# Performance work log

Hardware: AMD Instinct MI355X
Metric: run time of the kernel (lower is better)

Reference implementation:

```python
import jax, jax.numpy as jnp
import numpy as np

# ---- static hyperparameters (mirror init_kwargs) ----
L_MAX = 3
N_MAX_L = [8, 6, 4, 2]            # radial basis size per l (precomputer.n_max_l)
N_CHANNELS = 32                   # num_element_channels
K_MAX_L = [n * N_CHANNELS for n in N_MAX_L]   # [256, 192, 128, 64]
SH_SIZES = [2 * l + 1 for l in range(L_MAX + 1)]  # [1,3,5,7]
MP_SCALING = 0.1
NU_SCALING = 0.1
NU_MAX = 2                        # max_correlation_order_per_layer
N_LAYERS = 2                      # num_message_passing_layers

# Fixed CG coupling tensors for all valid (l1, l2, L) with |l1-l2|<=L<=min(l1+l2, L_MAX).
# (Deterministic stand-ins for real Clebsch-Gordan coefficients; same sparsity/coupling
# structure and identical in fwd and fwdbwd modules.)
_rng = np.random.RandomState(0)
CG = {}
for _l1 in range(L_MAX + 1):
    for _l2 in range(L_MAX + 1):
        for _L in range(abs(_l1 - _l2), min(_l1 + _l2, L_MAX) + 1):
            CG[(_l1, _l2, _L)] = jnp.asarray(
                (_rng.randn(2 * _l1 + 1, 2 * _l2 + 1, 2 * _L + 1) * 0.2).astype(np.float32))


def split_l(x, sizes):
    out, i = [], 0
    for s in sizes:
        out.append(x[:, i:i + s])
        i += s
    return out


def embed_centers(feats, emb):
    # feats[l]: [N, 2l+1, n_l*C]; multiply channel block c by per-atom embedding emb[:, c]
    C = emb.shape[1]
    out = []
    for f in feats:
        n, m, k = f.shape
        out.append((f.reshape(n, m, k // C, C) * emb[:, None, None, :]).reshape(n, m, k))
    return out


def tensor_product(A, B):
    # per-atom CG tensor product, channel-aligned with truncation to min k
    n = A[0].shape[0]
    out = [jnp.zeros((n, 2 * L + 1, K_MAX_L[L]), A[0].dtype) for L in range(L_MAX + 1)]
    for (l1, l2, L), cg in CG.items():
        kk = min(K_MAX_L[l1], K_MAX_L[l2], K_MAX_L[L])
        t = jnp.einsum('nak,nbk,abM->nMk', A[l1][:, :, :kk], B[l2][:, :, :kk], cg)
        out[L] = out[L].at[:, :, :kk].add(t)
    return out


def cg_iterate(feats):
    # CGIterator: nu_max-1 iterated tensor products with residual accumulation
    g = feats
    for _ in range(NU_MAX - 1):
        tp = tensor_product(g, feats)
        g = [g[l] + NU_SCALING * tp[l] for l in range(L_MAX + 1)]
    return g


def invariant_mp(rb_l, sh_l, centers, emb_nbr, n_atoms):
    # spherical expansion: scatter rb x sh x neighbor-embedding over pairs -> centers
    out = []
    for l in range(L_MAX + 1):
        # [P, 2l+1, n_l, C] -> [P, 2l+1, k_l]
        msg = sh_l[l][:, :, None, None] * rb_l[l][:, None, :, None] * emb_nbr[:, None, None, :]
        msg = msg.reshape(msg.shape[0], 2 * l + 1, -1)
        out.append(MP_SCALING * jax.ops.segment_sum(msg, centers, num_segments=n_atoms))
    return out


def equivariant_mp(rb_l, sh_l, centers, neighbors, feats, n_atoms):
    # pair messages: CG-couple radially weighted SH edge features with neighbor features
    edge = [sh_l[l] * rb_l[l].sum(-1, keepdims=True) for l in range(L_MAX + 1)]  # [P, 2l+1]
    out = [jnp.zeros((n_atoms, 2 * L + 1, K_MAX_L[L]), feats[0].dtype) for L in range(L_MAX + 1)]
    for (l1, l2, L), cg in CG.items():
        kk = min(K_MAX_L[l2], K_MAX_L[L])
        w = jnp.einsum('pa,abM->pbM', edge[l1], cg)        # [P, 2l2+1, 2L+1]
        fg = feats[l2][neighbors, :, :kk]                   # gather: [P, 2l2+1, kk]
        msg = jnp.einsum('pbM,pbk->pMk', w, fg)             # [P, 2L+1, kk]
        out[L] = out[L].at[:, :, :kk].add(
            MP_SCALING * jax.ops.segment_sum(msg, centers, num_segments=n_atoms))
    return out


def setup_inputs() -> dict:
    key = jax.random.key(0)
    ks = jax.random.split(key, 8)
    N, P = 5000, 100000
    return {
        'sh': jax.random.normal(ks[0], (P, sum(SH_SIZES)), dtype=jnp.float32),
        'rb': jax.random.uniform(ks[1], (P, sum(N_MAX_L)), dtype=jnp.float32),
        'emb_table': jax.random.normal(ks[2], (4, N_CHANNELS), dtype=jnp.float32),
        'w_energy': jax.random.normal(ks[3], (K_MAX_L[0], 1), dtype=jnp.float32) * 0.05,
        'b_energy': jax.random.normal(ks[4], (1,), dtype=jnp.float32),
        'species_idx': jax.random.randint(ks[5], (N,), 0, 4, dtype=jnp.int32),
        'centers': jax.random.randint(ks[6], (P,), 0, N, dtype=jnp.int32),
        'neighbors': jax.random.randint(ks[7], (P,), 0, N, dtype=jnp.int32),
    }


def reference(sh, rb, emb_table, w_energy, b_energy, species_idx, centers, neighbors):
    n_atoms = species_idx.shape[0]
    sh_l = split_l(sh * NU_SCALING, SH_SIZES)   # nu_scaling applied to spherical harmonics
    rb_l = split_l(rb, N_MAX_L)
    center_emb = emb_table[species_idx]          # [N, C]
    emb_nbr = center_emb[neighbors]              # [P, C]
    # invariant message passing -> spherical expansion, then first CG iteration
    feats = invariant_mp(rb_l, sh_l, centers, emb_nbr, n_atoms)
    feats = cg_iterate(feats)
    # remaining equivariant message-passing layers
    for _ in range(N_LAYERS - 1):
        ef = embed_centers(feats, center_emb)
        mp = equivariant_mp(rb_l, sh_l, centers, neighbors, ef, n_atoms)
        feats = cg_iterate(mp)
    feats = embed_centers(feats, center_emb)
    energies = feats[0] @ w_energy + b_energy    # [N, 1, 1]
    return energies
```

## Files before the change

kernel.cpp:

```cpp
#include <hip/hip_runtime.h>
#include <vector>
#include <cmath>
#include <cstdint>

constexpr int KLc[4]  = {256,192,128,64};
constexpr int NMLc[4] = {8,6,4,2};
constexpr int SHBc[5] = {0,1,4,9,16};
constexpr int RBBc[5] = {0,8,14,18,20};
constexpr int FBc[5]  = {0,256,832,1472,1920};
constexpr int NCMB = 34, CGTOT = 3436, FTOT = 1920;

struct Combos { int l1[NCMB], l2[NCMB], L[NCMB], cgoff[NCMB], kk[NCMB]; };
constexpr Combos make_combos(){
  Combos c{}; int n=0, cg=0;
  for(int a=0;a<=3;a++)for(int b=0;b<=3;b++){
    int lo=a>b?a-b:b-a, hi=(a+b<3)?(a+b):3;
    for(int L=lo;L<=hi;L++){
      c.l1[n]=a; c.l2[n]=b; c.L[n]=L; c.cgoff[n]=cg;
      int mx=a>b?a:b; if(L>mx) mx=L; c.kk[n]=KLc[mx];
      cg+=(2*a+1)*(2*b+1)*(2*L+1); n++;
    }
  }
  return c;
}
constexpr Combos CB = make_combos();
static_assert(CB.cgoff[NCMB-1] + 7*7*7 == CGTOT, "cg size");

struct Grp { int cnt[4]; int list[4][12]; };
constexpr Grp make_Lg(){ Grp g{}; for(int i=0;i<NCMB;i++){ int L=CB.L[i]; g.list[L][g.cnt[L]++]=i; } return g; }
constexpr Grp LG = make_Lg();

struct Rows { int sh[64], rb[64], off[64]; };
constexpr Rows make_rows(){ Rows r{}; int i=0;
  for(int l=0;l<4;l++)for(int m=0;m<2*l+1;m++)for(int n=0;n<NMLc[l];n++){
    r.sh[i]=SHBc[l]+m; r.rb[i]=RBBc[l]+n; r.off[i]=FBc[l]+m*KLc[l]+n*32; i++; }
  for(;i<64;i++){ r.sh[i]=0; r.rb[i]=0; r.off[i]=0; }
  return r; }
constexpr Rows RWS = make_rows();

constexpr int NSL=425, MAXS=107, MAXR=12, RPAD=149;

constexpr int iabs_(int x){ return x<0?-x:x; }
__host__ __device__ constexpr bool sl_valid(int l1,int l2,int kt){ return l2<=3-kt && iabs_(l1-l2)<=3-kt; }

__host__ __device__ constexpr int rb_base(int kt,int l1,int l2){
  int base=0;
  for(int p=0;p<4;p++)for(int q=0;q<4;q++){
    if(p==l1 && q==l2) return base;
    if(sl_valid(p,q,kt)) base += (2*p+1)*(2*q+1);
  }
  return base;
}

struct EqTab {
  int ns[4];
  unsigned char eidx[4][MAXS];
  unsigned char fidx[4][MAXS];
  short         srow[4][MAXS];
  unsigned char sph [4][MAXS];
  int nr[4];
  short roff[4][MAXR];
  int total;
};
constexpr EqTab make_eqtab(){
  EqTab T{}; int gidx=0;
  for(int l2=0;l2<4;l2++)for(int kt=0;kt<4-l2;kt++)for(int b=0;b<2*l2+1;b++){
    const int rowoff = FBc[l2] + b*KLc[l2] + kt*64;
    for(int l1=0;l1<4;l1++){
      if(!sl_valid(l1,l2,kt)) continue;
      for(int a=0;a<2*l1+1;a++){
        int g = (gidx*4)/NSL;
        int s = T.ns[g]++;
        T.eidx[g][s] = (unsigned char)(SHBc[l1]+a);
        int rbi = rb_base(kt,l1,l2) + a*(2*l2+1) + b;
        int ph, sr;
        if(kt==0){ if(l1<=2){ ph=0; sr=rbi; } else { ph=1; sr=rbi-144; } }
        else { ph=kt+1; sr=rbi; }
        T.sph[g][s]=(unsigned char)ph; T.srow[g][s]=(short)sr;
        int ri=-1;
        for(int r=0;r<T.nr[g];r++) if(T.roff[g][r]==(short)rowoff) ri=r;
        if(ri<0){ ri=T.nr[g]; T.roff[g][T.nr[g]++]=(short)rowoff; }
        T.fidx[g][s]=(unsigned char)ri;
        gidx++;
      }
    }
  }
  T.total=gidx;
  return T;
}
constexpr EqTab ET = make_eqtab();
static_assert(ET.total==NSL, "slice count");
static_assert(ET.ns[0]<=MAXS && ET.ns[1]<=MAXS && ET.ns[2]<=MAXS && ET.ns[3]<=MAXS, "MAXS");
static_assert(ET.nr[0]<=MAXR && ET.nr[1]<=MAXR && ET.nr[2]<=MAXR && ET.nr[3]<=MAXR, "MAXR");

struct CAsg { int cnt[4]; unsigned char ci[4][16]; };
constexpr CAsg make_casg(){
  CAsg C{}; bool used[NCMB]{}; int load[4]{};
  for(int it=0; it<NCMB; it++){
    int best=-1, bc=-1;
    for(int i=0;i<NCMB;i++) if(!used[i]){
      int c=(2*CB.l1[i]+1)*(2*CB.l2[i]+1)*(2*CB.L[i]+1);
      if(c>bc){bc=c;best=i;}
    }
    used[best]=true;
    int g=0; for(int j=1;j<4;j++) if(load[j]<load[g]) g=j;
    C.ci[g][C.cnt[g]++]=(unsigned char)best; load[g]+=bc;
  }
  return C;
}
constexpr CAsg CA = make_casg();
static_assert(CA.cnt[0]<=16 && CA.cnt[1]<=16 && CA.cnt[2]<=16 && CA.cnt[3]<=16, "CA cap");

__host__ __device__ constexpr bool combo_in_phase(int ci,int ph){
  int l1=CB.l1[ci], l2=CB.l2[ci], L=CB.L[ci];
  if(ph==0) return l1<=2;
  if(ph==1) return l1==3;
  int kt=ph-1;
  return (l2<=3-kt) && (L<=3-kt);
}
__host__ __device__ constexpr int phase_kt(int ph){ return ph<=1?0:ph-1; }
__host__ __device__ constexpr int phase_rbadj(int ph){ return ph==1?144:0; }

namespace nprng {
struct MT {
  uint32_t mt[624]; int mti; bool has_g; double g;
  void seed(uint32_t s){ for(int i=0;i<624;i++){ mt[i]=s; s=1812433253u*(s^(s>>30))+(uint32_t)i+1u; } mti=624; has_g=false; g=0.0; }
  uint32_t u32(){
    if(mti>=624){
      for(int i=0;i<624;i++){
        uint32_t y=(mt[i]&0x80000000u)|(mt[(i+1)%624]&0x7fffffffu);
        mt[i]=mt[(i+397)%624]^(y>>1)^((y&1u)?0x9908b0dfu:0u);
      }
      mti=0;
    }
    uint32_t y=mt[mti++];
    y^=y>>11; y^=(y<<7)&0x9d2c5680u; y^=(y<<15)&0xefc60000u; y^=y>>18;
    return y;
  }
  double dbl(){ uint32_t a=u32()>>5, b=u32()>>6; return (a*67108864.0+b)/9007199254740992.0; }
  double gauss(){
    if(has_g){ has_g=false; return g; }
    double f,x1,x2,r2;
    do{ x1=2.0*dbl()-1.0; x2=2.0*dbl()-1.0; r2=x1*x1+x2*x2; }while(r2>=1.0||r2==0.0);
    f=sqrt(-2.0*log(r2)/r2);
    g=f*x1; has_g=true; return f*x2;
  }
};
}
static std::vector<float> build_cg(){
  nprng::MT r; r.seed(0);
  std::vector<float> v; v.reserve(CGTOT);
  for(int l1=0;l1<=3;l1++)for(int l2=0;l2<=3;l2++){
    int lo = l1>l2? l1-l2 : l2-l1;
    int hi = (l1+l2<3)? (l1+l2) : 3;
    for(int L=lo;L<=hi;L++){
      int n=(2*l1+1)*(2*l2+1)*(2*L+1);
      for(int i=0;i<n;i++) v.push_back((float)(r.gauss()*0.2));
    }
  }
  return v;
}

__global__ __launch_bounds__(256) void k_cemb(const float* __restrict__ emb_table,
    const int* __restrict__ species, float* __restrict__ cemb, int* __restrict__ counts, int N){
  int i = blockIdx.x*256 + threadIdx.x;
  if(i < N) counts[i] = 0;
  if(i < N*32){ int n = i>>5, c = i&31; cemb[i] = emb_table[species[n]*32 + c]; }
}

__global__ __launch_bounds__(256) void k_hist(const int* __restrict__ centers, int* counts, int P){
  int i = blockIdx.x*256 + threadIdx.x;
  if(i < P) atomicAdd(&counts[centers[i]], 1);
}

__global__ __launch_bounds__(256) void k_scan(const int* __restrict__ counts,
    int* __restrict__ offsets, int* __restrict__ cursor, int N){
  __shared__ int part[256];
  const int t = threadIdx.x;
  const int CH = (N + 255)/256;
  const int lo = t*CH;
  int hi = (t+1)*CH; if(hi > N) hi = N;
  int s = 0;
  for(int i=lo;i<hi;i++) s += counts[i];
  part[t] = s; __syncthreads();
  const int own = s;
  for(int d=1; d<256; d<<=1){
    int v = (t>=d)? part[t-d] : 0;
    __syncthreads();
    part[t] += v;
    __syncthreads();
  }
  int run = part[t] - own;
  for(int i=lo;i<hi;i++){ offsets[i]=run; cursor[i]=run; run += counts[i]; }
  if(t==255) offsets[N] = part[255];
}

__global__ __launch_bounds__(256) void k_scatter(const int* __restrict__ centers,
    int* cursor, int* __restrict__ perm, int P){
  int i = blockIdx.x*256 + threadIdx.x;
  if(i < P){ int c = centers[i]; int pos = atomicAdd(&cursor[c], 1); perm[pos] = i; }
}

__global__ __launch_bounds__(256) void k_inv(const float* __restrict__ sh, const float* __restrict__ rb,
    const float* __restrict__ cemb, const int* __restrict__ nbrs, const int* __restrict__ offsets,
    const int* __restrict__ perm, float* __restrict__ feats){
  const int a = blockIdx.x, t = threadIdx.x;
  __shared__ float sh_s[8][16], rb_s[8][20], emb_s[8][32], shrb_s[8][60];
  const int c = t & 31, rg = t >> 5;
  float acc[8];
  #pragma unroll
  for(int j=0;j<8;j++) acc[j] = 0.f;
  const int beg = offsets[a], cnt = offsets[a+1]-beg;
  for(int jb=0; jb<cnt; jb+=8){
    __syncthreads();
    for(int u=t; u<8*36; u+=256){
      int j=u/36, i=u-36*j;
      if(jb+j<cnt){
        int p=perm[beg+jb+j];
        if(i<16) sh_s[j][i]=sh[p*16+i]*0.1f;
        else     rb_s[j][i-16]=rb[p*20+i-16];
      }
    }
    for(int u=t; u<8*32; u+=256){
      int j=u>>5, i=u&31;
      if(jb+j<cnt){ int nb=nbrs[perm[beg+jb+j]]; emb_s[j][i]=cemb[(size_t)nb*32+i]; }
    }
    __syncthreads();
    for(int u=t; u<8*60; u+=256){
      int j=u/60, r=u-60*j;
      if(jb+j<cnt) shrb_s[j][r] = sh_s[j][RWS.sh[r]] * rb_s[j][RWS.rb[r]];
    }
    __syncthreads();
    const int jm = (cnt-jb<8)?(cnt-jb):8;
    for(int j=0;j<jm;j++){
      const float e = emb_s[j][c];
      #pragma unroll
      for(int q=0;q<8;q++){ int r=rg+8*q; if(r<60) acc[q]=fmaf(shrb_s[j][r], e, acc[q]); }
    }
  }
  #pragma unroll
  for(int q=0;q<8;q++){
    int r = rg + 8*q;
    if(r < 60) feats[(size_t)a*FTOT + RWS.off[r] + c] = 0.1f * acc[q];
  }
}

__global__ __launch_bounds__(256) void k_tp(float* __restrict__ feats, const float* __restrict__ cg){
  const int a = blockIdx.x, t = threadIdx.x;
  __shared__ float f_s[FTOT];
  __shared__ float cg_s[CGTOT];
  float* fa = feats + (size_t)a*FTOT;
  for(int i=t;i<CGTOT;i+=256) cg_s[i] = cg[i];
  for(int i=t;i<FTOT;i+=256)  f_s[i]  = fa[i];
  __syncthreads();
  #pragma unroll
  for(int L=0; L<4; L++){
    const int KLL = KLc[L], nL = 2*L+1;
    const int nel = nL*KLL;
    for(int e=t; e<nel; e+=256){
      const int M = e / KLL, k = e - M*KLL;
      float acc = 0.f;
      #pragma unroll
      for(int gi=0; gi<LG.cnt[L]; gi++){
        const int ci = LG.list[L][gi];
        const int l1 = CB.l1[ci], l2 = CB.l2[ci];
        if(k < CB.kk[ci]){
          const int n2 = 2*l2+1;
          #pragma unroll
          for(int aa=0; aa<2*l1+1; aa++){
            const float Av = f_s[FBc[l1] + aa*KLc[l1] + k];
            #pragma unroll
            for(int b=0; b<n2; b++)
              acc += cg_s[CB.cgoff[ci] + (aa*n2+b)*nL + M] * (Av * f_s[FBc[l2] + b*KLc[l2] + k]);
          }
        }
      }
      fa[FBc[L] + M*KLL + k] = f_s[FBc[L] + M*KLL + k] + 0.1f*acc;
    }
  }
}

template<int G,int PH,int U>
__device__ __forceinline__ void contract_combos(const float* __restrict__ stageT,
    float* __restrict__ out_s, const float* __restrict__ cg, int lane){
  if constexpr (U < CA.cnt[G]) {
    constexpr int ci = CA.ci[G][U];
    if constexpr (combo_in_phase(ci,PH)) {
      constexpr int l1=CB.l1[ci], l2=CB.l2[ci], L=CB.L[ci];
      constexpr int n1=2*l1+1, n2=2*l2+1, nL=2*L+1;
      constexpr int kt=phase_kt(PH);
      constexpr int rbase = rb_base(kt,l1,l2) - phase_rbadj(PH);
      float oa[nL];
      #pragma unroll
      for(int M=0;M<nL;M++) oa[M]=0.f;
      #pragma unroll
      for(int aa=0;aa<n1;aa++){
        #pragma unroll
        for(int b=0;b<n2;b++){
          const float sv = stageT[lane*RPAD + rbase + aa*n2 + b];
          #pragma unroll
          for(int M=0;M<nL;M++)
            oa[M] = fmaf(cg[CB.cgoff[ci] + (aa*n2+b)*nL + M], sv, oa[M]);
        }
      }
      #pragma unroll
      for(int M=0;M<nL;M++)
        atomicAdd(&out_s[FBc[L] + M*KLc[L] + kt*64 + lane], oa[M]);
    }
    contract_combos<G,PH,U+1>(stageT,out_s,cg,lane);
  }
}

template<int G,int PH>
__device__ __forceinline__ void eq_phase(const float* acc, float* stageT, float* out_s,
    const float* __restrict__ cg, int lane){
  __syncthreads();
  #pragma unroll
  for(int s=0;s<ET.ns[G];s++){
    if(ET.sph[G][s]==PH) stageT[lane*RPAD + ET.srow[G][s]] = acc[s];
  }
  __syncthreads();
  contract_combos<G,PH,0>(stageT,out_s,cg,lane);
}

template<int G>
__device__ __forceinline__ void eq_group_main(
    const int a, const int t, const int lane,
    const float* __restrict__ sh, const float* __restrict__ rb,
    const float* __restrict__ cemb, const int* __restrict__ nbrs,
    const int* __restrict__ offsets, const int* __restrict__ perm,
    const float* __restrict__ featsA, float* __restrict__ featsB,
    const float* __restrict__ cg,
    float* stageT, float* out_s, float* edge_s, int* nb_s){
  constexpr int NS = ET.ns[G], NR = ET.nr[G];
  float acc[NS];
  #pragma unroll
  for(int s=0;s<NS;s++) acc[s]=0.f;
  for(int i=t;i<FTOT;i+=256) out_s[i]=0.f;
  const int beg = offsets[a], cnt = offsets[a+1]-beg;
  for(int jb=0; jb<cnt; jb+=8){
    __syncthreads();
    if(t < 128){
      int j=t>>4, i=t&15;
      if(jb+j<cnt){
        int p = perm[beg+jb+j];
        if(i==0) nb_s[j] = nbrs[p];
        int l = (i==0)?0:(i<4)?1:(i<9)?2:3;
        float s=0.f;
        for(int n=RBBc[l]; n<RBBc[l+1]; n++) s += rb[p*20+n];
        edge_s[j*16+i] = sh[p*16+i]*0.1f*s;
      }
    }
    __syncthreads();
    const int jm = (cnt-jb<8)?(cnt-jb):8;
    for(int j=0;j<jm;j++){
      const int nb = nb_s[j];
      const float ce = cemb[(size_t)nb*32 + (lane&31)];
      const float* fp = featsA + (size_t)nb*FTOT + lane;
      float fgv[NR];
      #pragma unroll
      for(int r=0;r<NR;r++) fgv[r] = fp[ET.roff[G][r]] * ce;
      float ed[16];
      #pragma unroll
      for(int q=0;q<4;q++){
        float4 v = *(const float4*)(edge_s + j*16 + q*4);
        ed[q*4]=v.x; ed[q*4+1]=v.y; ed[q*4+2]=v.z; ed[q*4+3]=v.w;
      }
      #pragma unroll
      for(int s=0;s<NS;s++)
        acc[s] = fmaf(ed[ET.eidx[G][s]], fgv[ET.fidx[G][s]], acc[s]);
    }
  }
  eq_phase<G,0>(acc,stageT,out_s,cg,lane);
  eq_phase<G,1>(acc,stageT,out_s,cg,lane);
  eq_phase<G,2>(acc,stageT,out_s,cg,lane);
  eq_phase<G,3>(acc,stageT,out_s,cg,lane);
  eq_phase<G,4>(acc,stageT,out_s,cg,lane);
  __syncthreads();
  float* ob = featsB + (size_t)a*FTOT;
  for(int i=t;i<FTOT;i+=256) ob[i] = 0.1f*out_s[i];
}

__global__ __launch_bounds__(256,3) void k_eq2(const float* __restrict__ sh, const float* __restrict__ rb,
    const float* __restrict__ cemb, const int* __restrict__ nbrs, const int* __restrict__ offsets,
    const int* __restrict__ perm, const float* __restrict__ featsA, float* __restrict__ featsB,
    const float* __restrict__ cg){
  __shared__ float stageT[64*RPAD];
  __shared__ float out_s[FTOT];
  __shared__ float edge_s[8*16];
  __shared__ int   nb_s[8];
  const int a = blockIdx.x, t = threadIdx.x, lane = t&63, g = t>>6;
  switch(g){
    case 0: eq_group_main<0>(a,t,lane,sh,rb,cemb,nbrs,offsets,perm,featsA,featsB,cg,stageT,out_s,edge_s,nb_s); break;
    case 1: eq_group_main<1>(a,t,lane,sh,rb,cemb,nbrs,offsets,perm,featsA,featsB,cg,stageT,out_s,edge_s,nb_s); break;
    case 2: eq_group_main<2>(a,t,lane,sh,rb,cemb,nbrs,offsets,perm,featsA,featsB,cg,stageT,out_s,edge_s,nb_s); break;
    default: eq_group_main<3>(a,t,lane,sh,rb,cemb,nbrs,offsets,perm,featsA,featsB,cg,stageT,out_s,edge_s,nb_s); break;
  }
}

__global__ __launch_bounds__(256) void k_energy(const float* __restrict__ feats,
    const float* __restrict__ cemb, const float* __restrict__ wE, const float* __restrict__ bE,
    float* __restrict__ out, int N){
  const int wid = threadIdx.x >> 6, lane = threadIdx.x & 63;
  const int a = blockIdx.x*4 + wid;
  if(a >= N) return;
  const float e = cemb[(size_t)a*32 + (lane & 31)];
  float s = 0.f;
  for(int k=lane; k<256; k+=64) s += feats[(size_t)a*FTOT + k] * e * wE[k];
  #pragma unroll
  for(int off=32; off; off>>=1) s += __shfl_down(s, off, 64);
  if(lane == 0) out[a] = s + bE[0];
}

extern "C" void kernel_launch(void* const* d_in, const int* in_sizes, int n_in,
                              void* d_out, int out_size, void* d_ws, size_t ws_size,
                              hipStream_t stream){
  const float* sh        = (const float*)d_in[0];
  const float* rb        = (const float*)d_in[1];
  const float* emb_table = (const float*)d_in[2];
  const float* wE        = (const float*)d_in[3];
  const float* bE        = (const float*)d_in[4];
  const int*   species   = (const int*)d_in[5];
  const int*   centers   = (const int*)d_in[6];
  const int*   nbrs      = (const int*)d_in[7];
  const int N = in_sizes[5];
  const int P = in_sizes[6];

  char* ws = (char*)d_ws; size_t off = 0;
  auto carve = [&](size_t bytes)->void*{
    void* p = ws + off; off = (off + bytes + 255) & ~(size_t)255; return p;
  };
  float* cg_d    = (float*)carve((size_t)CGTOT*4);
  float* cemb    = (float*)carve((size_t)N*32*4);
  int*   counts  = (int*)  carve((size_t)N*4);
  int*   offsets = (int*)  carve((size_t)(N+1)*4);
  int*   cursor  = (int*)  carve((size_t)N*4);
  int*   perm    = (int*)  carve((size_t)P*4);
  float* featsA  = (float*)carve((size_t)N*FTOT*4);
  float* featsB  = (float*)carve((size_t)N*FTOT*4);
  (void)ws_size; (void)n_in; (void)out_size;

  static const std::vector<float> cg_host = build_cg();
  hipMemcpyAsync(cg_d, cg_host.data(), (size_t)CGTOT*4, hipMemcpyHostToDevice, stream);

  k_cemb   <<<(N*32 + 255)/256, 256, 0, stream>>>(emb_table, species, cemb, counts, N);
  k_hist   <<<(P + 255)/256,    256, 0, stream>>>(centers, counts, P);
  k_scan   <<<1,                256, 0, stream>>>(counts, offsets, cursor, N);
  k_scatter<<<(P + 255)/256,    256, 0, stream>>>(centers, cursor, perm, P);
  k_inv    <<<N,                256, 0, stream>>>(sh, rb, cemb, nbrs, offsets, perm, featsA);
  k_tp     <<<N,                256, 0, stream>>>(featsA, cg_d);
  k_eq2    <<<N,                256, 0, stream>>>(sh, rb, cemb, nbrs, offsets, perm, featsA, featsB, cg_d);
  k_tp     <<<N,                256, 0, stream>>>(featsB, cg_d);
  k_energy <<<(N + 3)/4,        256, 0, stream>>>(featsB, cemb, wE, bE, (float*)d_out, N);
}
```

Measured before the change: 965.4 us.

## Split equivariant kernel into eight waves, prefetch neighbor features, read CG uniformly

The equivariant message-passing kernel now runs 8 wavefronts per atom (512 threads) instead of 4, so each wave holds about half as many accumulator slices and combos. Neighbor feature rows are software-prefetched one neighbor ahead into registers, and edges are staged 16 at a time instead of 8. The tensor-product kernel drops its shared-memory copy of the CG table and reads it from global memory through a wave-uniform index, making those loads scalar. Risks include more register pressure from the prefetch buffers, higher shared-memory contention with more waves, and scalar-cache misses on CG reads.

```diff
diff --git a/kernel.cpp b/kernel.cpp
--- a/kernel.cpp
+++ b/kernel.cpp
@@ -38,7 +38,7 @@
   return r; }
 constexpr Rows RWS = make_rows();
 
-constexpr int NSL=425, MAXS=107, MAXR=12, RPAD=149;
+constexpr int NSL=425, NG=8, MAXS=56, MAXR=12, RPAD=149;
 
 constexpr int iabs_(int x){ return x<0?-x:x; }
 __host__ __device__ constexpr bool sl_valid(int l1,int l2,int kt){ return l2<=3-kt && iabs_(l1-l2)<=3-kt; }
@@ -53,13 +53,13 @@
 }
 
 struct EqTab {
-  int ns[4];
-  unsigned char eidx[4][MAXS];
-  unsigned char fidx[4][MAXS];
-  short         srow[4][MAXS];
-  unsigned char sph [4][MAXS];
-  int nr[4];
-  short roff[4][MAXR];
+  int ns[NG];
+  unsigned char eidx[NG][MAXS];
+  unsigned char fidx[NG][MAXS];
+  short         srow[NG][MAXS];
+  unsigned char sph [NG][MAXS];
+  int nr[NG];
+  short roff[NG][MAXR];
   int total;
 };
 constexpr EqTab make_eqtab(){
@@ -69,7 +69,7 @@
     for(int l1=0;l1<4;l1++){
       if(!sl_valid(l1,l2,kt)) continue;
       for(int a=0;a<2*l1+1;a++){
-        int g = (gidx*4)/NSL;
+        int g = (gidx*NG)/NSL;
         int s = T.ns[g]++;
         T.eidx[g][s] = (unsigned char)(SHBc[l1]+a);
         int rbi = rb_base(kt,l1,l2) + a*(2*l2+1) + b;
@@ -90,12 +90,14 @@
 }
 constexpr EqTab ET = make_eqtab();
 static_assert(ET.total==NSL, "slice count");
-static_assert(ET.ns[0]<=MAXS && ET.ns[1]<=MAXS && ET.ns[2]<=MAXS && ET.ns[3]<=MAXS, "MAXS");
-static_assert(ET.nr[0]<=MAXR && ET.nr[1]<=MAXR && ET.nr[2]<=MAXR && ET.nr[3]<=MAXR, "MAXR");
-
-struct CAsg { int cnt[4]; unsigned char ci[4][16]; };
+constexpr bool chk_ns(){ for(int g=0;g<NG;g++) if(ET.ns[g]>MAXS) return false; return true; }
+constexpr bool chk_nr(){ for(int g=0;g<NG;g++) if(ET.nr[g]>MAXR) return false; return true; }
+static_assert(chk_ns(), "MAXS");
+static_assert(chk_nr(), "MAXR");
+
+struct CAsg { int cnt[NG]; unsigned char ci[NG][8]; };
 constexpr CAsg make_casg(){
-  CAsg C{}; bool used[NCMB]{}; int load[4]{};
+  CAsg C{}; bool used[NCMB]{}; int load[NG]{};
   for(int it=0; it<NCMB; it++){
     int best=-1, bc=-1;
     for(int i=0;i<NCMB;i++) if(!used[i]){
@@ -103,13 +105,14 @@
       if(c>bc){bc=c;best=i;}
     }
     used[best]=true;
-    int g=0; for(int j=1;j<4;j++) if(load[j]<load[g]) g=j;
+    int g=0; for(int j=1;j<NG;j++) if(load[j]<load[g]) g=j;
     C.ci[g][C.cnt[g]++]=(unsigned char)best; load[g]+=bc;
   }
   return C;
 }
 constexpr CAsg CA = make_casg();
-static_assert(CA.cnt[0]<=16 && CA.cnt[1]<=16 && CA.cnt[2]<=16 && CA.cnt[3]<=16, "CA cap");
+constexpr bool chk_ca(){ for(int g=0;g<NG;g++) if(CA.cnt[g]>8) return false; return true; }
+static_assert(chk_ca(), "CA cap");
 
 __host__ __device__ constexpr bool combo_in_phase(int ci,int ph){
   int l1=CB.l1[ci], l2=CB.l2[ci], L=CB.L[ci];
@@ -245,12 +248,13 @@
   }
 }
 
+__device__ __forceinline__ float cg_u(const float* __restrict__ cg, int idx){
+  return cg[__builtin_amdgcn_readfirstlane(idx)];
+}
 __global__ __launch_bounds__(256) void k_tp(float* __restrict__ feats, const float* __restrict__ cg){
   const int a = blockIdx.x, t = threadIdx.x;
   __shared__ float f_s[FTOT];
-  __shared__ float cg_s[CGTOT];
   float* fa = feats + (size_t)a*FTOT;
-  for(int i=t;i<CGTOT;i+=256) cg_s[i] = cg[i];
   for(int i=t;i<FTOT;i+=256)  f_s[i]  = fa[i];
   __syncthreads();
   #pragma unroll
@@ -271,7 +275,7 @@
             const float Av = f_s[FBc[l1] + aa*KLc[l1] + k];
             #pragma unroll
             for(int b=0; b<n2; b++)
-              acc += cg_s[CB.cgoff[ci] + (aa*n2+b)*nL + M] * (Av * f_s[FBc[l2] + b*KLc[l2] + k]);
+              acc += cg_u(cg, CB.cgoff[ci] + (aa*n2+b)*nL + M) * (Av * f_s[FBc[l2] + b*KLc[l2] + k]);
           }
         }
       }
@@ -336,11 +340,19 @@
   float acc[NS];
   #pragma unroll
   for(int s=0;s<NS;s++) acc[s]=0.f;
-  for(int i=t;i<FTOT;i+=256) out_s[i]=0.f;
+  for(int i=t;i<FTOT;i+=512) out_s[i]=0.f;
   const int beg = offsets[a], cnt = offsets[a+1]-beg;
-  for(int jb=0; jb<cnt; jb+=8){
-    __syncthreads();
-    if(t < 128){
+  float fg_c[NR], ce_c = 0.f;
+  if(cnt > 0){
+    const int nb0 = nbrs[perm[beg]];
+    ce_c = cemb[(size_t)nb0*32 + (lane&31)];
+    const float* fp = featsA + (size_t)nb0*FTOT + lane;
+    #pragma unroll
+    for(int r=0;r<NR;r++) fg_c[r] = fp[ET.roff[G][r]];
+  }
+  for(int jb=0; jb<cnt; jb+=16){
+    __syncthreads();
+    if(t < 256){
       int j=t>>4, i=t&15;
       if(jb+j<cnt){
         int p = perm[beg+jb+j];
@@ -352,23 +364,35 @@
       }
     }
     __syncthreads();
-    const int jm = (cnt-jb<8)?(cnt-jb):8;
+    const int jm = (cnt-jb<16)?(cnt-jb):16;
     for(int j=0;j<jm;j++){
-      const int nb = nb_s[j];
-      const float ce = cemb[(size_t)nb*32 + (lane&31)];
-      const float* fp = featsA + (size_t)nb*FTOT + lane;
-      float fgv[NR];
-      #pragma unroll
-      for(int r=0;r<NR;r++) fgv[r] = fp[ET.roff[G][r]] * ce;
+      int nb_n = 0; bool have_n = true;
+      if(j+1 < jm)            nb_n = nb_s[j+1];
+      else if(jb+16 < cnt)    nb_n = nbrs[perm[beg+jb+16]];
+      else                    have_n = false;
+      float fg_n[NR], ce_n = 0.f;
+      {
+        const int nbl = have_n ? nb_n : 0;
+        ce_n = cemb[(size_t)nbl*32 + (lane&31)];
+        const float* fp = featsA + (size_t)nbl*FTOT + lane;
+        #pragma unroll
+        for(int r=0;r<NR;r++) fg_n[r] = fp[ET.roff[G][r]];
+      }
       float ed[16];
       #pragma unroll
       for(int q=0;q<4;q++){
         float4 v = *(const float4*)(edge_s + j*16 + q*4);
         ed[q*4]=v.x; ed[q*4+1]=v.y; ed[q*4+2]=v.z; ed[q*4+3]=v.w;
       }
+      float fgc[NR];
+      #pragma unroll
+      for(int r=0;r<NR;r++) fgc[r] = fg_c[r]*ce_c;
       #pragma unroll
       for(int s=0;s<NS;s++)
-        acc[s] = fmaf(ed[ET.eidx[G][s]], fgv[ET.fidx[G][s]], acc[s]);
+        acc[s] = fmaf(ed[ET.eidx[G][s]], fgc[ET.fidx[G][s]], acc[s]);
+      #pragma unroll
+      for(int r=0;r<NR;r++) fg_c[r] = fg_n[r];
+      ce_c = ce_n;
     }
   }
   eq_phase<G,0>(acc,stageT,out_s,cg,lane);
@@ -378,23 +402,27 @@
   eq_phase<G,4>(acc,stageT,out_s,cg,lane);
   __syncthreads();
   float* ob = featsB + (size_t)a*FTOT;
-  for(int i=t;i<FTOT;i+=256) ob[i] = 0.1f*out_s[i];
-}
-
-__global__ __launch_bounds__(256,3) void k_eq2(const float* __restrict__ sh, const float* __restrict__ rb,
+  for(int i=t;i<FTOT;i+=512) ob[i] = 0.1f*out_s[i];
+}
+
+__global__ __launch_bounds__(512,4) void k_eq2(const float* __restrict__ sh, const float* __restrict__ rb,
     const float* __restrict__ cemb, const int* __restrict__ nbrs, const int* __restrict__ offsets,
     const int* __restrict__ perm, const float* __restrict__ featsA, float* __restrict__ featsB,
     const float* __restrict__ cg){
   __shared__ float stageT[64*RPAD];
   __shared__ float out_s[FTOT];
-  __shared__ float edge_s[8*16];
-  __shared__ int   nb_s[8];
+  __shared__ float edge_s[16*16];
+  __shared__ int   nb_s[16];
   const int a = blockIdx.x, t = threadIdx.x, lane = t&63, g = t>>6;
   switch(g){
     case 0: eq_group_main<0>(a,t,lane,sh,rb,cemb,nbrs,offsets,perm,featsA,featsB,cg,stageT,out_s,edge_s,nb_s); break;
     case 1: eq_group_main<1>(a,t,lane,sh,rb,cemb,nbrs,offsets,perm,featsA,featsB,cg,stageT,out_s,edge_s,nb_s); break;
     case 2: eq_group_main<2>(a,t,lane,sh,rb,cemb,nbrs,offsets,perm,featsA,featsB,cg,stageT,out_s,edge_s,nb_s); break;
-    default: eq_group_main<3>(a,t,lane,sh,rb,cemb,nbrs,offsets,perm,featsA,featsB,cg,stageT,out_s,edge_s,nb_s); break;
+    case 3: eq_group_main<3>(a,t,lane,sh,rb,cemb,nbrs,offsets,perm,featsA,featsB,cg,stageT,out_s,edge_s,nb_s); break;
+    case 4: eq_group_main<4>(a,t,lane,sh,rb,cemb,nbrs,offsets,perm,featsA,featsB,cg,stageT,out_s,edge_s,nb_s); break;
+    case 5: eq_group_main<5>(a,t,lane,sh,rb,cemb,nbrs,offsets,perm,featsA,featsB,cg,stageT,out_s,edge_s,nb_s); break;
+    case 6: eq_group_main<6>(a,t,lane,sh,rb,cemb,nbrs,offsets,perm,featsA,featsB,cg,stageT,out_s,edge_s,nb_s); break;
+    default: eq_group_main<7>(a,t,lane,sh,rb,cemb,nbrs,offsets,perm,featsA,featsB,cg,stageT,out_s,edge_s,nb_s); break;
   }
 }
 
@@ -449,7 +477,7 @@
   k_scatter<<<(P + 255)/256,    256, 0, stream>>>(centers, cursor, perm, P);
   k_inv    <<<N,                256, 0, stream>>>(sh, rb, cemb, nbrs, offsets, perm, featsA);
   k_tp     <<<N,                256, 0, stream>>>(featsA, cg_d);
-  k_eq2    <<<N,                256, 0, stream>>>(sh, rb, cemb, nbrs, offsets, perm, featsA, featsB, cg_d);
+  k_eq2    <<<N,                512, 0, stream>>>(sh, rb, cemb, nbrs, offsets, perm, featsA, featsB, cg_d);
   k_tp     <<<N,                256, 0, stream>>>(featsB, cg_d);
   k_energy <<<(N + 3)/4,        256, 0, stream>>>(featsB, cemb, wE, bE, (float*)d_out, N);
 }
```

Result: faster. 936.2 us (-3.0%).

## Restructure equivariant message passing with async LDS neighbor prefetch and 8 wave groups

Applied to the files above, without the earlier changes.

Rewrites k_eq2 to use 512 threads split into 8 wave groups driven by constexpr job tables in constant memory. Neighbor feature rows are prefetched into a 4-slot LDS ring with global_load_lds. Per-edge sh*rb products are precomputed by a new k_edge kernel in center-sorted order. The center embedding multiply moves into k_tp's output, so neighbor gathers and k_energy no longer apply it, and k_tp reads CG coefficients from global memory instead of staging them in LDS. This aims to cut redundant per-neighbor loads and hide gather latency, at the cost of a 64-register accumulator per thread, LDS atomics and an extra kernel launch.

```diff
diff --git a/kernel.cpp b/kernel.cpp
--- a/kernel.cpp
+++ b/kernel.cpp
@@ -38,11 +38,8 @@
   return r; }
 constexpr Rows RWS = make_rows();
 
-constexpr int NSL=425, MAXS=107, MAXR=12, RPAD=149;
-
 constexpr int iabs_(int x){ return x<0?-x:x; }
 __host__ __device__ constexpr bool sl_valid(int l1,int l2,int kt){ return l2<=3-kt && iabs_(l1-l2)<=3-kt; }
-
 __host__ __device__ constexpr int rb_base(int kt,int l1,int l2){
   int base=0;
   for(int p=0;p<4;p++)for(int q=0;q<4;q++){
@@ -52,74 +49,101 @@
   return base;
 }
 
-struct EqTab {
-  int ns[4];
-  unsigned char eidx[4][MAXS];
-  unsigned char fidx[4][MAXS];
-  short         srow[4][MAXS];
-  unsigned char sph [4][MAXS];
-  int nr[4];
-  short roff[4][MAXR];
-  int total;
+constexpr int NG=8, CHUNK=64, SPITCH=145, JUNKROW=144, RINGF=1024, NJMAX=64;
+constexpr int REGTOT=11264;
+
+struct V7 {
+  short roff[NG*4];
+  unsigned short drow[NG*64];
+  unsigned char dumpmask[NG];
+  unsigned short jcg[NJMAX];
+  unsigned char  jrb[NJMAX], jn12[NJMAX], jnl[NJMAX];
+  unsigned short jout[NJMAX], jos[NJMAX];
+  short jix[NG*6];
+  int njobs;
 };
-constexpr EqTab make_eqtab(){
-  EqTab T{}; int gidx=0;
+constexpr V7 make_v7(){
+  V7 T{};
+  int rl2[30],rbb[30],rkt[30],rns[30]; int nrw=0;
   for(int l2=0;l2<4;l2++)for(int kt=0;kt<4-l2;kt++)for(int b=0;b<2*l2+1;b++){
-    const int rowoff = FBc[l2] + b*KLc[l2] + kt*64;
-    for(int l1=0;l1<4;l1++){
-      if(!sl_valid(l1,l2,kt)) continue;
-      for(int a=0;a<2*l1+1;a++){
-        int g = (gidx*4)/NSL;
-        int s = T.ns[g]++;
-        T.eidx[g][s] = (unsigned char)(SHBc[l1]+a);
-        int rbi = rb_base(kt,l1,l2) + a*(2*l2+1) + b;
-        int ph, sr;
-        if(kt==0){ if(l1<=2){ ph=0; sr=rbi; } else { ph=1; sr=rbi-144; } }
-        else { ph=kt+1; sr=rbi; }
-        T.sph[g][s]=(unsigned char)ph; T.srow[g][s]=(short)sr;
-        int ri=-1;
-        for(int r=0;r<T.nr[g];r++) if(T.roff[g][r]==(short)rowoff) ri=r;
-        if(ri<0){ ri=T.nr[g]; T.roff[g][T.nr[g]++]=(short)rowoff; }
-        T.fidx[g][s]=(unsigned char)ri;
-        gidx++;
-      }
-    }
-  }
-  T.total=gidx;
+    int l1max=l2+3-kt; if(l1max>3) l1max=3;
+    rl2[nrw]=l2; rbb[nrw]=b; rkt[nrw]=kt; rns[nrw]=SHBc[l1max+1]; nrw++;
+  }
+  int ord[30]; int no=0;
+  for(int pass=0; pass<4; pass++){
+    int want=(pass==0)?16:(pass==1)?9:(pass==2)?4:1;
+    for(int i=0;i<nrw;i++) if(rns[i]==want) ord[no++]=i;
+  }
+  int asgG[30], asgS[30];
+  for(int i=0;i<nrw;i++){
+    if(i<24){ asgG[ord[i]]=i%8; asgS[ord[i]]=i/8; }
+    else    { asgG[ord[i]]=i-24; asgS[ord[i]]=3; }
+  }
+  for(int i=0;i<NG*4;i++) T.roff[i]=0;
+  for(int r=0;r<nrw;r++)
+    T.roff[asgG[r]*4+asgS[r]] = (short)(FBc[rl2[r]] + rbb[r]*KLc[rl2[r]] + rkt[r]*64);
+  for(int g=0;g<NG;g++){ bool h3=false; for(int r=0;r<nrw;r++) if(asgG[r]==g&&asgS[r]==3) h3=true;
+    if(!h3) T.roff[g*4+3]=T.roff[g*4+2]; }
+  for(int i=0;i<NG*64;i++) T.drow[i]=0xF000;
+  for(int r=0;r<nrw;r++){
+    const int g=asgG[r], s=asgS[r], l2=rl2[r], b=rbb[r], kt=rkt[r];
+    for(int e=0;e<rns[r];e++){
+      const int l1=(e==0)?0:(e<4)?1:(e<9)?2:3;
+      const int a=e-SHBc[l1];
+      const int ph=(kt==0)?(l1<=2?0:1):kt+1;
+      const int srow=rb_base(kt,l1,l2)+a*(2*l2+1)+b-(ph==1?144:0);
+      T.drow[g*64+s*16+e]=(unsigned short)(srow|(ph<<12));
+      T.dumpmask[g]|=(unsigned char)(1<<ph);
+    }
+  }
+  int cgrp[NCMB]={};
+  { bool used[NCMB]={}; long load[NG]={};
+    for(int it=0;it<NCMB;it++){
+      int best=-1; long bc=-1;
+      for(int i=0;i<NCMB;i++) if(!used[i]){
+        int mx=CB.l2[i]>CB.L[i]?CB.l2[i]:CB.L[i];
+        long c=(long)(2*CB.l1[i]+1)*(2*CB.l2[i]+1)*(2*CB.L[i]+1)*(4-mx);
+        if(c>bc){bc=c;best=i;}
+      }
+      used[best]=true;
+      int g=0; for(int j=1;j<NG;j++) if(load[j]<load[g]) g=j;
+      cgrp[best]=g; load[g]+=1;
+    }
+  }
+  int nj=0;
+  for(int g=0;g<NG;g++){
+    for(int ph=0;ph<5;ph++){
+      T.jix[g*6+ph]=(short)nj;
+      for(int ci=0;ci<NCMB;ci++){
+        if(cgrp[ci]!=g) continue;
+        const int l1=CB.l1[ci], l2=CB.l2[ci], L=CB.L[ci];
+        int ok=0, kt=0;
+        if(ph==0){ ok=(l1<=2); kt=0; }
+        else if(ph==1){ ok=(l1==3); kt=0; }
+        else { kt=ph-1; ok=(l2<=3-kt)&&(L<=3-kt); }
+        if(!ok) continue;
+        T.jcg[nj]=(unsigned short)CB.cgoff[ci];
+        T.jrb[nj]=(unsigned char)(rb_base(kt,l1,l2)-(ph==1?144:0));
+        T.jn12[nj]=(unsigned char)((2*l1+1)*(2*l2+1));
+        T.jnl[nj]=(unsigned char)(2*L+1);
+        T.jout[nj]=(unsigned short)(FBc[L]+kt*64);
+        T.jos[nj]=(unsigned short)KLc[L];
+        nj++;
+      }
+    }
+    T.jix[g*6+5]=(short)nj;
+  }
+  T.njobs=nj;
   return T;
 }
-constexpr EqTab ET = make_eqtab();
-static_assert(ET.total==NSL, "slice count");
-static_assert(ET.ns[0]<=MAXS && ET.ns[1]<=MAXS && ET.ns[2]<=MAXS && ET.ns[3]<=MAXS, "MAXS");
-static_assert(ET.nr[0]<=MAXR && ET.nr[1]<=MAXR && ET.nr[2]<=MAXR && ET.nr[3]<=MAXR, "MAXR");
-
-struct CAsg { int cnt[4]; unsigned char ci[4][16]; };
-constexpr CAsg make_casg(){
-  CAsg C{}; bool used[NCMB]{}; int load[4]{};
-  for(int it=0; it<NCMB; it++){
-    int best=-1, bc=-1;
-    for(int i=0;i<NCMB;i++) if(!used[i]){
-      int c=(2*CB.l1[i]+1)*(2*CB.l2[i]+1)*(2*CB.L[i]+1);
-      if(c>bc){bc=c;best=i;}
-    }
-    used[best]=true;
-    int g=0; for(int j=1;j<4;j++) if(load[j]<load[g]) g=j;
-    C.ci[g][C.cnt[g]++]=(unsigned char)best; load[g]+=bc;
-  }
-  return C;
-}
-constexpr CAsg CA = make_casg();
-static_assert(CA.cnt[0]<=16 && CA.cnt[1]<=16 && CA.cnt[2]<=16 && CA.cnt[3]<=16, "CA cap");
-
-__host__ __device__ constexpr bool combo_in_phase(int ci,int ph){
-  int l1=CB.l1[ci], l2=CB.l2[ci], L=CB.L[ci];
-  if(ph==0) return l1<=2;
-  if(ph==1) return l1==3;
-  int kt=ph-1;
-  return (l2<=3-kt) && (L<=3-kt);
-}
-__host__ __device__ constexpr int phase_kt(int ph){ return ph<=1?0:ph-1; }
-__host__ __device__ constexpr int phase_rbadj(int ph){ return ph==1?144:0; }
+static_assert(make_v7().njobs <= NJMAX, "NJMAX");
+__constant__ V7 V7T = make_v7();
+
+constexpr int vmimm(int n){ return (n&15) | ((n>>4)<<14) | (7<<4) | (15<<8); }
+__device__ __forceinline__ void gload_lds16(const float* g, float* l){
+  __builtin_amdgcn_global_load_lds((const __attribute__((address_space(1))) void*)g,
+                                   (__attribute__((address_space(3))) void*)l, 16, 0, 0);
+}
 
 namespace nprng {
 struct MT {
@@ -151,8 +175,7 @@
   nprng::MT r; r.seed(0);
   std::vector<float> v; v.reserve(CGTOT);
   for(int l1=0;l1<=3;l1++)for(int l2=0;l2<=3;l2++){
-    int lo = l1>l2? l1-l2 : l2-l1;
-    int hi = (l1+l2<3)? (l1+l2) : 3;
+    int lo=l1>l2?l1-l2:l2-l1, hi=(l1+l2<3)?(l1+l2):3;
     for(int L=lo;L<=hi;L++){
       int n=(2*l1+1)*(2*l2+1)*(2*L+1);
       for(int i=0;i<n;i++) v.push_back((float)(r.gauss()*0.2));
@@ -201,6 +224,20 @@
   if(i < P){ int c = centers[i]; int pos = atomicAdd(&cursor[c], 1); perm[pos] = i; }
 }
 
+__global__ __launch_bounds__(256) void k_edge(const float* __restrict__ sh, const float* __restrict__ rb,
+    const int* __restrict__ perm, const int* __restrict__ nbrs,
+    float* __restrict__ edgeP, int* __restrict__ nbP, int P){
+  int u = blockIdx.x*256 + threadIdx.x;
+  if(u >= P*16) return;
+  const int ip = u>>4, i = u&15;
+  const int p = perm[ip];
+  const int l = (i==0)?0:(i<4)?1:(i<9)?2:3;
+  float s = 0.f;
+  for(int n=RBBc[l]; n<RBBc[l+1]; n++) s += rb[p*20+n];
+  edgeP[u] = sh[p*16+i]*0.1f*s;
+  if(i==0) nbP[ip] = nbrs[p];
+}
+
 __global__ __launch_bounds__(256) void k_inv(const float* __restrict__ sh, const float* __restrict__ rb,
     const float* __restrict__ cemb, const int* __restrict__ nbrs, const int* __restrict__ offsets,
     const int* __restrict__ perm, float* __restrict__ feats){
@@ -245,12 +282,13 @@
   }
 }
 
-__global__ __launch_bounds__(256) void k_tp(float* __restrict__ feats, const float* __restrict__ cg){
+__global__ __launch_bounds__(256) void k_tp(float* __restrict__ feats, const float* __restrict__ cg,
+    const float* __restrict__ cemb){
   const int a = blockIdx.x, t = threadIdx.x;
   __shared__ float f_s[FTOT];
-  __shared__ float cg_s[CGTOT];
+  __shared__ float cemb_s[32];
   float* fa = feats + (size_t)a*FTOT;
-  for(int i=t;i<CGTOT;i+=256) cg_s[i] = cg[i];
+  if(t < 32) cemb_s[t] = cemb[(size_t)a*32 + t];
   for(int i=t;i<FTOT;i+=256)  f_s[i]  = fa[i];
   __syncthreads();
   #pragma unroll
@@ -271,142 +309,119 @@
             const float Av = f_s[FBc[l1] + aa*KLc[l1] + k];
             #pragma unroll
             for(int b=0; b<n2; b++)
-              acc += cg_s[CB.cgoff[ci] + (aa*n2+b)*nL + M] * (Av * f_s[FBc[l2] + b*KLc[l2] + k]);
+              acc += cg[CB.cgoff[ci] + (aa*n2+b)*nL + M] * (Av * f_s[FBc[l2] + b*KLc[l2] + k]);
           }
         }
       }
-      fa[FBc[L] + M*KLL + k] = f_s[FBc[L] + M*KLL + k] + 0.1f*acc;
-    }
-  }
-}
-
-template<int G,int PH,int U>
-__device__ __forceinline__ void contract_combos(const float* __restrict__ stageT,
-    float* __restrict__ out_s, const float* __restrict__ cg, int lane){
-  if constexpr (U < CA.cnt[G]) {
-    constexpr int ci = CA.ci[G][U];
-    if constexpr (combo_in_phase(ci,PH)) {
-      constexpr int l1=CB.l1[ci], l2=CB.l2[ci], L=CB.L[ci];
-      constexpr int n1=2*l1+1, n2=2*l2+1, nL=2*L+1;
-      constexpr int kt=phase_kt(PH);
-      constexpr int rbase = rb_base(kt,l1,l2) - phase_rbadj(PH);
-      float oa[nL];
+      fa[FBc[L] + M*KLL + k] = (f_s[FBc[L] + M*KLL + k] + 0.1f*acc) * cemb_s[k & 31];
+    }
+  }
+}
+
+template<int NL> __device__ __forceinline__ void job_k(const float* __restrict__ slane,
+    float* __restrict__ out_s, const float* __restrict__ cg, const int j, const int lane){
+  const int cgb=V7T.jcg[j], rbB=V7T.jrb[j], n12=V7T.jn12[j], outB=V7T.jout[j], ostr=V7T.jos[j];
+  float oa[NL];
+  #pragma unroll
+  for(int M=0;M<NL;M++) oa[M]=0.f;
+  const float* sp = slane + rbB;
+  const float* cp = cg + cgb;
+  for(int o=0;o<n12;o++){
+    const float sv = sp[o];
+    #pragma unroll
+    for(int M=0;M<NL;M++) oa[M]=fmaf(cp[o*NL+M], sv, oa[M]);
+  }
+  #pragma unroll
+  for(int M=0;M<NL;M++) atomicAdd(&out_s[outB + M*ostr + lane], oa[M]);
+}
+
+__global__ __launch_bounds__(512,4) void k_eq2(const float* __restrict__ edgeP, const int* __restrict__ nbP,
+    const int* __restrict__ offsets, const float* __restrict__ featsA, float* __restrict__ featsB,
+    const float* __restrict__ cg){
+  __shared__ float region[REGTOT];
+  const int a = blockIdx.x, t = threadIdx.x, lane = t&63;
+  const int g = __builtin_amdgcn_readfirstlane(t>>6);
+  float* ring   = region + g*RINGF;
+  float* edge_s = region + NG*RINGF;
+  int*   nbs    = (int*)(region + NG*RINGF + CHUNK*16);
+  const int rsel = lane>>4;
+  const int roffl = V7T.roff[g*4+rsel] + ((lane&15)<<2);
+  float acc[64];
+  #pragma unroll
+  for(int i=0;i<64;i++) acc[i]=0.f;
+  const int beg = offsets[a], cnt = offsets[a+1]-beg;
+
+  for(int c0=0; c0<cnt; c0+=CHUNK){
+    const int clen = (cnt-c0<CHUNK)?(cnt-c0):CHUNK;
+    __builtin_amdgcn_s_waitcnt(vmimm(0));
+    __syncthreads();
+    for(int u=t; u<CHUNK*16; u+=512){
+      const int j=u>>4, i=u&15;
+      edge_s[u] = (j<clen) ? edgeP[((size_t)(beg+c0+j)<<4)+i] : 0.f;
+    }
+    if(t < CHUNK){ int jj=t; if(jj>clen-1) jj=clen-1; nbs[t]=nbP[beg+c0+jj]; }
+    __syncthreads();
+    gload_lds16(featsA + (size_t)nbs[0]*FTOT + roffl, ring + 0*256);
+    gload_lds16(featsA + (size_t)nbs[clen>1?1:0]*FTOT + roffl, ring + 1*256);
+    for(int j=0; j<clen; j++){
+      int jn=j+2; if(jn>clen-1) jn=clen-1;
+      gload_lds16(featsA + (size_t)nbs[jn]*FTOT + roffl, ring + ((j+2)&3)*256);
+      __builtin_amdgcn_s_waitcnt(vmimm(2));
+      const float* ep = edge_s + j*16;
+      const float* rs = ring + (j&3)*256;
+      const float fv0=rs[lane], fv1=rs[64+lane], fv2=rs[128+lane], fv3=rs[192+lane];
       #pragma unroll
-      for(int M=0;M<nL;M++) oa[M]=0.f;
+      for(int q4=0;q4<4;q4++){
+        const float4 e4 = *(const float4*)(ep + q4*4);
+        #pragma unroll
+        for(int r=0;r<4;r++){
+          const float fvr = (r==0)?fv0:(r==1)?fv1:(r==2)?fv2:fv3;
+          acc[r*16+q4*4+0] = fmaf(e4.x, fvr, acc[r*16+q4*4+0]);
+          acc[r*16+q4*4+1] = fmaf(e4.y, fvr, acc[r*16+q4*4+1]);
+          acc[r*16+q4*4+2] = fmaf(e4.z, fvr, acc[r*16+q4*4+2]);
+          acc[r*16+q4*4+3] = fmaf(e4.w, fvr, acc[r*16+q4*4+3]);
+        }
+      }
+    }
+  }
+  __builtin_amdgcn_s_waitcnt(vmimm(0));
+  __syncthreads();
+  float* stage = region;
+  float* out_s = region + 64*SPITCH;
+  for(int i=t;i<FTOT;i+=512) out_s[i]=0.f;
+  float* slane = stage + lane*SPITCH;
+  for(int ph=0; ph<5; ph++){
+    __syncthreads();
+    if(V7T.dumpmask[g] & (1<<ph)){
       #pragma unroll
-      for(int aa=0;aa<n1;aa++){
-        #pragma unroll
-        for(int b=0;b<n2;b++){
-          const float sv = stageT[lane*RPAD + rbase + aa*n2 + b];
-          #pragma unroll
-          for(int M=0;M<nL;M++)
-            oa[M] = fmaf(cg[CB.cgoff[ci] + (aa*n2+b)*nL + M], sv, oa[M]);
-        }
-      }
-      #pragma unroll
-      for(int M=0;M<nL;M++)
-        atomicAdd(&out_s[FBc[L] + M*KLc[L] + kt*64 + lane], oa[M]);
-    }
-    contract_combos<G,PH,U+1>(stageT,out_s,cg,lane);
-  }
-}
-
-template<int G,int PH>
-__device__ __forceinline__ void eq_phase(const float* acc, float* stageT, float* out_s,
-    const float* __restrict__ cg, int lane){
-  __syncthreads();
-  #pragma unroll
-  for(int s=0;s<ET.ns[G];s++){
-    if(ET.sph[G][s]==PH) stageT[lane*RPAD + ET.srow[G][s]] = acc[s];
-  }
-  __syncthreads();
-  contract_combos<G,PH,0>(stageT,out_s,cg,lane);
-}
-
-template<int G>
-__device__ __forceinline__ void eq_group_main(
-    const int a, const int t, const int lane,
-    const float* __restrict__ sh, const float* __restrict__ rb,
-    const float* __restrict__ cemb, const int* __restrict__ nbrs,
-    const int* __restrict__ offsets, const int* __restrict__ perm,
-    const float* __restrict__ featsA, float* __restrict__ featsB,
-    const float* __restrict__ cg,
-    float* stageT, float* out_s, float* edge_s, int* nb_s){
-  constexpr int NS = ET.ns[G], NR = ET.nr[G];
-  float acc[NS];
-  #pragma unroll
-  for(int s=0;s<NS;s++) acc[s]=0.f;
-  for(int i=t;i<FTOT;i+=256) out_s[i]=0.f;
-  const int beg = offsets[a], cnt = offsets[a+1]-beg;
-  for(int jb=0; jb<cnt; jb+=8){
-    __syncthreads();
-    if(t < 128){
-      int j=t>>4, i=t&15;
-      if(jb+j<cnt){
-        int p = perm[beg+jb+j];
-        if(i==0) nb_s[j] = nbrs[p];
-        int l = (i==0)?0:(i<4)?1:(i<9)?2:3;
-        float s=0.f;
-        for(int n=RBBc[l]; n<RBBc[l+1]; n++) s += rb[p*20+n];
-        edge_s[j*16+i] = sh[p*16+i]*0.1f*s;
-      }
-    }
-    __syncthreads();
-    const int jm = (cnt-jb<8)?(cnt-jb):8;
-    for(int j=0;j<jm;j++){
-      const int nb = nb_s[j];
-      const float ce = cemb[(size_t)nb*32 + (lane&31)];
-      const float* fp = featsA + (size_t)nb*FTOT + lane;
-      float fgv[NR];
-      #pragma unroll
-      for(int r=0;r<NR;r++) fgv[r] = fp[ET.roff[G][r]] * ce;
-      float ed[16];
-      #pragma unroll
-      for(int q=0;q<4;q++){
-        float4 v = *(const float4*)(edge_s + j*16 + q*4);
-        ed[q*4]=v.x; ed[q*4+1]=v.y; ed[q*4+2]=v.z; ed[q*4+3]=v.w;
-      }
-      #pragma unroll
-      for(int s=0;s<NS;s++)
-        acc[s] = fmaf(ed[ET.eidx[G][s]], fgv[ET.fidx[G][s]], acc[s]);
-    }
-  }
-  eq_phase<G,0>(acc,stageT,out_s,cg,lane);
-  eq_phase<G,1>(acc,stageT,out_s,cg,lane);
-  eq_phase<G,2>(acc,stageT,out_s,cg,lane);
-  eq_phase<G,3>(acc,stageT,out_s,cg,lane);
-  eq_phase<G,4>(acc,stageT,out_s,cg,lane);
+      for(int e=0;e<64;e++){
+        const int dv = V7T.drow[g*64+e];
+        const int dst = ((dv>>12)==ph) ? (dv & 0xFFF) : JUNKROW;
+        slane[dst] = acc[e];
+      }
+    }
+    __syncthreads();
+    for(int j=V7T.jix[g*6+ph]; j<V7T.jix[g*6+ph+1]; j++){
+      const int nL = V7T.jnl[j];
+      if(nL==1)      job_k<1>(slane,out_s,cg,j,lane);
+      else if(nL==3) job_k<3>(slane,out_s,cg,j,lane);
+      else if(nL==5) job_k<5>(slane,out_s,cg,j,lane);
+      else           job_k<7>(slane,out_s,cg,j,lane);
+    }
+  }
   __syncthreads();
   float* ob = featsB + (size_t)a*FTOT;
-  for(int i=t;i<FTOT;i+=256) ob[i] = 0.1f*out_s[i];
-}
-
-__global__ __launch_bounds__(256,3) void k_eq2(const float* __restrict__ sh, const float* __restrict__ rb,
-    const float* __restrict__ cemb, const int* __restrict__ nbrs, const int* __restrict__ offsets,
-    const int* __restrict__ perm, const float* __restrict__ featsA, float* __restrict__ featsB,
-    const float* __restrict__ cg){
-  __shared__ float stageT[64*RPAD];
-  __shared__ float out_s[FTOT];
-  __shared__ float edge_s[8*16];
-  __shared__ int   nb_s[8];
-  const int a = blockIdx.x, t = threadIdx.x, lane = t&63, g = t>>6;
-  switch(g){
-    case 0: eq_group_main<0>(a,t,lane,sh,rb,cemb,nbrs,offsets,perm,featsA,featsB,cg,stageT,out_s,edge_s,nb_s); break;
-    case 1: eq_group_main<1>(a,t,lane,sh,rb,cemb,nbrs,offsets,perm,featsA,featsB,cg,stageT,out_s,edge_s,nb_s); break;
-    case 2: eq_group_main<2>(a,t,lane,sh,rb,cemb,nbrs,offsets,perm,featsA,featsB,cg,stageT,out_s,edge_s,nb_s); break;
-    default: eq_group_main<3>(a,t,lane,sh,rb,cemb,nbrs,offsets,perm,featsA,featsB,cg,stageT,out_s,edge_s,nb_s); break;
-  }
+  for(int i=t;i<FTOT;i+=512) ob[i] = 0.1f*out_s[i];
 }
 
 __global__ __launch_bounds__(256) void k_energy(const float* __restrict__ feats,
-    const float* __restrict__ cemb, const float* __restrict__ wE, const float* __restrict__ bE,
+    const float* __restrict__ wE, const float* __restrict__ bE,
     float* __restrict__ out, int N){
   const int wid = threadIdx.x >> 6, lane = threadIdx.x & 63;
   const int a = blockIdx.x*4 + wid;
   if(a >= N) return;
-  const float e = cemb[(size_t)a*32 + (lane & 31)];
   float s = 0.f;
-  for(int k=lane; k<256; k+=64) s += feats[(size_t)a*FTOT + k] * e * wE[k];
+  for(int k=lane; k<256; k+=64) s += feats[(size_t)a*FTOT + k] * wE[k];
   #pragma unroll
   for(int off=32; off; off>>=1) s += __shfl_down(s, off, 64);
   if(lane == 0) out[a] = s + bE[0];
@@ -436,6 +451,8 @@
   int*   offsets = (int*)  carve((size_t)(N+1)*4);
   int*   cursor  = (int*)  carve((size_t)N*4);
   int*   perm    = (int*)  carve((size_t)P*4);
+  int*   nbP     = (int*)  carve((size_t)P*4);
+  float* edgeP   = (float*)carve((size_t)P*16*4);
   float* featsA  = (float*)carve((size_t)N*FTOT*4);
   float* featsB  = (float*)carve((size_t)N*FTOT*4);
   (void)ws_size; (void)n_in; (void)out_size;
@@ -447,9 +464,10 @@
   k_hist   <<<(P + 255)/256,    256, 0, stream>>>(centers, counts, P);
   k_scan   <<<1,                256, 0, stream>>>(counts, offsets, cursor, N);
   k_scatter<<<(P + 255)/256,    256, 0, stream>>>(centers, cursor, perm, P);
+  k_edge   <<<(P*16 + 255)/256, 256, 0, stream>>>(sh, rb, perm, nbrs, edgeP, nbP, P);
   k_inv    <<<N,                256, 0, stream>>>(sh, rb, cemb, nbrs, offsets, perm, featsA);
-  k_tp     <<<N,                256, 0, stream>>>(featsA, cg_d);
-  k_eq2    <<<N,                256, 0, stream>>>(sh, rb, cemb, nbrs, offsets, perm, featsA, featsB, cg_d);
-  k_tp     <<<N,                256, 0, stream>>>(featsB, cg_d);
-  k_energy <<<(N + 3)/4,        256, 0, stream>>>(featsB, cemb, wE, bE, (float*)d_out, N);
-}
+  k_tp     <<<N,                256, 0, stream>>>(featsA, cg_d, cemb);
+  k_eq2    <<<N,                512, 0, stream>>>(edgeP, nbP, offsets, featsA, featsB, cg_d);
+  k_tp     <<<N,                256, 0, stream>>>(featsB, cg_d, cemb);
+  k_energy <<<(N + 3)/4,        256, 0, stream>>>(featsB, wE, bE, (float*)d_out, N);
+}
```

New measurement: 1.196 ms. 1.24x slower.
